# Optimization experiments

Measured on AMD Instinct MI355X. Metric: run time of the kernel, lower is better.

The kernel has to match this reference:

```python
import jax, jax.numpy as jnp
import numpy as np

# ---- config (YOLOv4-style, TRAIN_SIZE=608, P2..P5) ----
STRIDES = (4.0, 8.0, 16.0, 32.0)
ANCHORS = np.array([
    [[12, 16], [19, 36], [40, 28], [36, 75]],
    [[36, 75], [76, 55], [72, 146], [142, 110]],
    [[72, 146], [142, 110], [192, 243], [459, 401]],
    [[142, 110], [192, 243], [300, 300], [459, 401]],
], dtype=np.float32)  # [LEVELS, NUM_ANCHORS, 2]
MAX_PROP = 100
SCORE_THRESH = 0.25
IOU_THRESH = 0.5


def decode_prediction(p, anchors, stride):
    # p: [b, A, h, w, 6] -> [b, A*h*w, 5] with xyxy + score
    b, A, h, w, _ = p.shape
    txy, twh, conf, cls = p[..., :2], p[..., 2:4], p[..., 4:5], p[..., 5:6]
    gx, gy = jnp.meshgrid(jnp.arange(w, dtype=p.dtype), jnp.arange(h, dtype=p.dtype))
    grid = jnp.stack([gx, gy], axis=-1)[None, None]  # [1,1,h,w,2]
    xy = (jax.nn.sigmoid(txy) + grid) * stride
    wh = jnp.exp(twh) * anchors[None, :, None, None, :]
    score = jax.nn.sigmoid(conf) * jax.nn.sigmoid(cls)
    x1y1 = xy - 0.5 * wh
    x2y2 = xy + 0.5 * wh
    out = jnp.concatenate([x1y1, x2y2, score], axis=-1)  # [b,A,h,w,5]
    return out.reshape(b, A * h * w, 5)


def _iou_one_vs_all(box, boxes):
    # box: [4], boxes: [N,4] (xyxy)
    lt = jnp.maximum(box[:2], boxes[:, :2])
    rb = jnp.minimum(box[2:], boxes[:, 2:])
    wh = jnp.maximum(rb - lt, 0.0)
    inter = wh[:, 0] * wh[:, 1]
    a1 = jnp.maximum(box[2] - box[0], 0.0) * jnp.maximum(box[3] - box[1], 0.0)
    a2 = jnp.maximum(boxes[:, 2] - boxes[:, 0], 0.0) * jnp.maximum(boxes[:, 3] - boxes[:, 1], 0.0)
    return inter / (a1 + a2 - inter + 1e-9)


def _nms_single(boxes, scores):
    # greedy NMS, padded to MAX_PROP with zero rows
    s0 = jnp.where(scores >= SCORE_THRESH, scores, 0.0)

    def step(s, _):
        i = jnp.argmax(s)
        sc = s[i]
        box = boxes[i]
        keep = sc > 0.0
        row = jnp.where(keep, jnp.concatenate([box, sc[None]]), jnp.zeros(5, boxes.dtype))
        iou = _iou_one_vs_all(box, boxes)
        s = jnp.where((iou > IOU_THRESH) & keep, 0.0, s)
        s = s.at[i].set(0.0)
        return s, row

    _, props = jax.lax.scan(step, s0, None, length=MAX_PROP)
    return props  # [MAX_PROP, 5]


def entry_stop_gradients(t, mask):
    # gradient flows only through entries where mask==1
    return jax.lax.stop_gradient(t) * (1.0 - mask) + t * mask


def _forward(p2, p3, p4, p5):
    anchors = jnp.asarray(ANCHORS)
    d2 = decode_prediction(p2, anchors[0], STRIDES[0])
    d3 = decode_prediction(p3, anchors[1], STRIDES[1])
    d4 = decode_prediction(p4, anchors[2], STRIDES[2])
    d5 = decode_prediction(p5, anchors[3], STRIDES[3])
    proposals = jnp.concatenate([d2, d3, d4, d5], axis=1)  # [b, N, 5]
    proposals = jax.vmap(lambda pr: _nms_single(pr[:, :4], pr[:, 4]))(proposals)  # [b, MAX_PROP, 5]
    mask = (jnp.sum(proposals[..., :4], axis=-1) != 0.0).astype(proposals.dtype)[..., None]
    return entry_stop_gradients(proposals, mask)


def setup_inputs() -> dict:
    key = jax.random.key(0)
    k2, k3, k4, k5 = jax.random.split(key, 4)
    b, A, ch = 32, 4, 6
    return {
        "p2": jax.random.normal(k2, (b, A, 152, 152, ch), dtype=jnp.float32),
        "p3": jax.random.normal(k3, (b, A, 76, 76, ch), dtype=jnp.float32),
        "p4": jax.random.normal(k4, (b, A, 38, 38, ch), dtype=jnp.float32),
        "p5": jax.random.normal(k5, (b, A, 19, 19, ch), dtype=jnp.float32),
    }


def reference(p2, p3, p4, p5):
    return _forward(p2, p3, p4, p5)
```

## Files before the change

### kernel.cpp

```cpp
#include <hip/hip_runtime.h>
#include <cstdint>
#include <cstddef>

typedef unsigned int u32;
typedef unsigned long long u64;

#define NTOT 122740
#define NPAIR 61370
#define KTOP 1024
#define WIN  256
#define NBIN 4096
#define SCORE_T 0.25f
#define TBITS 0x3E800000u
#define HSPLIT_BITS 0x3EFFF000u
#define CSTRIDE 64
#define CAP_H 40960
#define CAP_L 20480

#define F4TOT 184110
#define F4B3 138624
#define F4B4 173280
#define F4B5 181944

#define WS_SORTED 8192
#define WS_CANDH  270336
#define WS_CANDL  10756096

__device__ __forceinline__ float sigm(float x) { return 1.0f / (1.0f + expf(-x)); }

__device__ __forceinline__ int score_bin(u32 bits) {
  return min(4095, 1 + (int)((bits - TBITS) >> 12));
}

__device__ __forceinline__ u64 shfl_u64(u64 x, int src) {
  int lo = __shfl((int)(u32)x, src, 64);
  int hi = __shfl((int)(u32)(x >> 32), src, 64);
  return ((u64)(u32)hi << 32) | (u32)lo;
}

__device__ __forceinline__ void score_pair(int P, int b,
    const float* __restrict__ p2, const float* __restrict__ p3,
    const float* __restrict__ p4, const float* __restrict__ p5,
    u32& b0, u32& b1, u32& gi0, u32& gi1)
{
  int t0 = 2 * P;
  const float* p; int l0, LN;
  if (t0 < 92416)       { p = p2; l0 = t0;          LN = 92416; }
  else if (t0 < 115520) { p = p3; l0 = t0 - 92416;  LN = 23104; }
  else if (t0 < 121296) { p = p4; l0 = t0 - 115520; LN = 5776;  }
  else                  { p = p5; l0 = t0 - 121296; LN = 1444;  }
  const float* q = p + ((size_t)b * LN + (size_t)l0) * 6;
  float4 v1 = *(const float4*)(q + 4);
  float4 v2 = *(const float4*)(q + 8);
  float s0 = sigm(v1.x) * sigm(v1.y);
  float s1 = sigm(v2.z) * sigm(v2.w);
  b0 = (s0 >= SCORE_T) ? __float_as_uint(s0) : 0u;
  b1 = (s1 >= SCORE_T) ? __float_as_uint(s1) : 0u;
  gi0 = (u32)t0; gi1 = (u32)(t0 + 1);
}

__device__ float4 decode_box_from_gidx(u32 gidx, int b,
    const float* __restrict__ p2, const float* __restrict__ p3,
    const float* __restrict__ p4, const float* __restrict__ p5)
{
  const float* p; int t, H, W; float stride;
  float aw0, ah0, aw1, ah1, aw2, ah2, aw3, ah3;
  if (gidx < 92416u) {
    p = p2 + (size_t)b * 92416 * 6; t = (int)gidx; H = 152; W = 152; stride = 4.0f;
    aw0=12.f; ah0=16.f; aw1=19.f; ah1=36.f; aw2=40.f; ah2=28.f; aw3=36.f; ah3=75.f;
  } else if (gidx < 115520u) {
    p = p3 + (size_t)b * 23104 * 6; t = (int)(gidx - 92416u); H = 76; W = 76; stride = 8.0f;
    aw0=36.f; ah0=75.f; aw1=76.f; ah1=55.f; aw2=72.f; ah2=146.f; aw3=142.f; ah3=110.f;
  } else if (gidx < 121296u) {
    p = p4 + (size_t)b * 5776 * 6; t = (int)(gidx - 115520u); H = 38; W = 38; stride = 16.0f;
    aw0=72.f; ah0=146.f; aw1=142.f; ah1=110.f; aw2=192.f; ah2=243.f; aw3=459.f; ah3=401.f;
  } else {
    p = p5 + (size_t)b * 1444 * 6; t = (int)(gidx - 121296u); H = 19; W = 19; stride = 32.0f;
    aw0=142.f; ah0=110.f; aw1=192.f; ah1=243.f; aw2=300.f; ah2=300.f; aw3=459.f; ah3=401.f;
  }
  int HW = H * W;
  int a = t / HW;
  int r = t - a * HW;
  int y = r / W;
  int x = r - y * W;
  const float* q = p + (size_t)t * 6;
  float2 t01 = *(const float2*)(q + 0);
  float2 t23 = *(const float2*)(q + 2);
  float cx = (sigm(t01.x) + (float)x) * stride;
  float cy = (sigm(t01.y) + (float)y) * stride;
  float aw = (a == 0) ? aw0 : (a == 1) ? aw1 : (a == 2) ? aw2 : aw3;
  float ah = (a == 0) ? ah0 : (a == 1) ? ah1 : (a == 2) ? ah2 : ah3;
  float bw = expf(t23.x) * aw;
  float bh = expf(t23.y) * ah;
  return make_float4(cx - 0.5f * bw, cy - 0.5f * bh, cx + 0.5f * bw, cy + 0.5f * bh);
}

__device__ __forceinline__ bool iou_gt(float4 A, float4 B) {
  float ltx = fmaxf(A.x, B.x), lty = fmaxf(A.y, B.y);
  float rbx = fminf(A.z, B.z), rby = fminf(A.w, B.w);
  float w = fmaxf(rbx - ltx, 0.0f), h = fmaxf(rby - lty, 0.0f);
  float inter = w * h;
  float a1 = fmaxf(A.z - A.x, 0.0f) * fmaxf(A.w - A.y, 0.0f);
  float a2 = fmaxf(B.z - B.x, 0.0f) * fmaxf(B.w - B.y, 0.0f);
  float iou = inter / (a1 + a2 - inter + 1e-9f);
  return iou > 0.5f;
}

__global__ __launch_bounds__(256)
void decode_kernel(const float* __restrict__ p2, const float* __restrict__ p3,
                   const float* __restrict__ p4, const float* __restrict__ p5,
                   u32* __restrict__ counters,
                   uint2* __restrict__ candH, uint2* __restrict__ candL)
{
  __shared__ float4 sbuf4[768];
  __shared__ uint2 stH[512];
  __shared__ uint2 stL[512];
  __shared__ u32 s_cH, s_cL, s_bH, s_bL;
  const int tid = threadIdx.x;
  const int b = blockIdx.y;
  if (tid == 0) { s_cH = 0u; s_cL = 0u; }

  const float4* q2 = (const float4*)p2;
  const float4* q3 = (const float4*)p3;
  const float4* q4 = (const float4*)p4;
  const float4* q5 = (const float4*)p5;

  const int f4base = blockIdx.x * 768;
  #pragma unroll
  for (int j = 0; j < 3; ++j) {
    int idx4 = f4base + j * 256 + tid;
    if (idx4 < F4TOT) {
      const float4* src;
      if (idx4 < F4B3)      src = q2 + (size_t)b * 138624 + idx4;
      else if (idx4 < F4B4) src = q3 + (size_t)b * 34656  + (idx4 - F4B3);
      else if (idx4 < F4B5) src = q4 + (size_t)b * 8664   + (idx4 - F4B4);
      else                  src = q5 + (size_t)b * 2166   + (idx4 - F4B5);
      sbuf4[j * 256 + tid] = *src;
    }
  }
  __syncthreads();

  const float* sbuf = (const float*)sbuf4;
  const int rbase = blockIdx.x * 512;
  #pragma unroll
  for (int k = 0; k < 2; ++k) {
    int lr = 2 * tid + k;
    int rg = rbase + lr;
    if (rg < NTOT) {
      float2 cc = *(const float2*)&sbuf[lr * 6 + 4];
      float s = sigm(cc.x) * sigm(cc.y);
      if (s >= SCORE_T) {
        u32 bits = __float_as_uint(s);
        bool H = (bits >= HSPLIT_BITS);
        u32 pos = atomicAdd(H ? &s_cH : &s_cL, 1u);
        if (pos < 512u) (H ? stH : stL)[pos] = make_uint2(bits, (u32)rg);
      }
    }
  }
  __syncthreads();
  if (tid == 0) {
    if (s_cH) s_bH = atomicAdd(&counters[(size_t)b * CSTRIDE],     s_cH);
    if (s_cL) s_bL = atomicAdd(&counters[(size_t)b * CSTRIDE + 1], s_cL);
  }
  __syncthreads();
  uint2* gH = candH + (size_t)b * CAP_H;
  uint2* gL = candL + (size_t)b * CAP_L;
  const u32 mH = min(s_cH, 512u), mL = min(s_cL, 512u);
  for (u32 i = tid; i < mH; i += 256) { u32 d = s_bH + i; if (d < (u32)CAP_H) gH[d] = stH[i]; }
  for (u32 i = tid; i < mL; i += 256) { u32 d = s_bL + i; if (d < (u32)CAP_L) gL[d] = stL[i]; }
}

__global__ __launch_bounds__(1024, 1)
void sort_kernel(const u32* __restrict__ counters_in, u32* __restrict__ counters,
                 const uint2* __restrict__ candH, const uint2* __restrict__ candL,
                 const float* __restrict__ p2, const float* __restrict__ p3,
                 const float* __restrict__ p4, const float* __restrict__ p5,
                 u64* __restrict__ sortedK)
{
  const int b = blockIdx.x;
  const int tid = threadIdx.x;

  __shared__ u32 sstart[NBIN];
  __shared__ u32 scur[NBIN];
  __shared__ u64 skey[KTOP];
  __shared__ int s_B, s_n;

  const u32 nHc = counters_in[(size_t)b * CSTRIDE];
  const u32 nLc = counters_in[(size_t)b * CSTRIDE + 1];
  const bool readL = (nHc < (u32)KTOP);
  const bool fb = (nHc > (u32)CAP_H) || (readL && nLc > (u32)CAP_L);

  for (int i = tid; i < NBIN; i += 1024) scur[i] = 0u;
  __syncthreads();

  if (!fb) {
    const uint2* gH = candH + (size_t)b * CAP_H;
    for (u32 i = tid; i < nHc; i += 1024) atomicAdd(&scur[score_bin(gH[i].x)], 1u);
    if (readL) {
      const uint2* gL = candL + (size_t)b * CAP_L;
      for (u32 i = tid; i < nLc; i += 1024) atomicAdd(&scur[score_bin(gL[i].x)], 1u);
    }
  } else {
    for (int P = tid; P < NPAIR; P += 1024) {
      u32 b0, b1, gi0, gi1;
      score_pair(P, b, p2, p3, p4, p5, b0, b1, gi0, gi1);
      if (b0) atomicAdd(&scur[score_bin(b0)], 1u);
      if (b1) atomicAdd(&scur[score_bin(b1)], 1u);
    }
  }
  __syncthreads();

  if (tid < 64) {
    u32 h[64];
    #pragma unroll
    for (int k = 0; k < 64; ++k) h[k] = scur[tid * 64 + k];
    u32 lsum = 0;
    #pragma unroll
    for (int k = 0; k < 64; ++k) lsum += h[k];
    u32 S = lsum;
    #pragma unroll
    for (int off = 1; off < 64; off <<= 1) {
      u32 v = (u32)__shfl_down((int)S, off, 64);
      if (tid + off < 64) S += v;
    }
    u32 c = S - lsum;
    int Bv = -1; u32 nv = 0;
    for (int k = 63; k >= 0; --k) {
      sstart[tid * 64 + k] = c;
      c += h[k];
      if (c <= (u32)KTOP) { Bv = tid * 64 + k; nv = c; }
    }
    u32 pk = (Bv < 0) ? 0xFFFFFFFFu : (((u32)Bv << 12) | nv);
    #pragma unroll
    for (int off = 32; off >= 1; off >>= 1) {
      u32 o = (u32)__shfl_down((int)pk, off, 64);
      if (tid + off < 64) pk = min(pk, o);
    }
    if (tid == 0) {
      if (pk == 0xFFFFFFFFu) { s_B = 4095; s_n = KTOP; }
      else { s_B = max((int)(pk >> 12), 1); s_n = (int)(pk & 0xFFFu); }
    }
  }
  __syncthreads();
  const int B = s_B;
  const int n = min(s_n, KTOP);

  for (int i = tid; i < NBIN; i += 1024) scur[i] = sstart[i];
  __syncthreads();

  if (!fb) {
    const uint2* gH = candH + (size_t)b * CAP_H;
    for (u32 i = tid; i < nHc; i += 1024) {
      uint2 e = gH[i];
      int bin = score_bin(e.x);
      if (bin >= B) {
        u32 slot = atomicAdd(&scur[bin], 1u);
        if (slot < (u32)KTOP) skey[slot] = ((u64)e.x << 32) | (u32)(~e.y);
      }
    }
    if (readL) {
      const uint2* gL = candL + (size_t)b * CAP_L;
      for (u32 i = tid; i < nLc; i += 1024) {
        uint2 e = gL[i];
        int bin = score_bin(e.x);
        if (bin >= B) {
          u32 slot = atomicAdd(&scur[bin], 1u);
          if (slot < (u32)KTOP) skey[slot] = ((u64)e.x << 32) | (u32)(~e.y);
        }
      }
    }
  } else {
    for (int P = tid; P < NPAIR; P += 1024) {
      u32 b0, b1, gi0, gi1;
      score_pair(P, b, p2, p3, p4, p5, b0, b1, gi0, gi1);
      if (b0) { int bin = score_bin(b0);
        if (bin >= B) { u32 slot = atomicAdd(&scur[bin], 1u);
          if (slot < (u32)KTOP) skey[slot] = ((u64)b0 << 32) | (u32)(~gi0); } }
      if (b1) { int bin = score_bin(b1);
        if (bin >= B) { u32 slot = atomicAdd(&scur[bin], 1u);
          if (slot < (u32)KTOP) skey[slot] = ((u64)b1 << 32) | (u32)(~gi1); } }
    }
  }
  __syncthreads();

  u64* dst = sortedK + (size_t)b * KTOP;
  for (int s = tid; s < n; s += 1024) {
    u64 k = skey[s];
    int bin = score_bin((u32)(k >> 32));
    int st = (int)sstart[bin];
    int en = (int)scur[bin];
    u32 r = 0;
    for (int j = st; j < en; ++j) r += (skey[j] > k) ? 1u : 0u;
    dst[st + r] = k;
  }
  if (tid == 0) counters[(size_t)b * CSTRIDE + 8] = (u32)n;
}

__global__ __launch_bounds__(1024, 1)
void nms_kernel(const u32* __restrict__ counters, const u64* __restrict__ sortedK,
                const float* __restrict__ p2, const float* __restrict__ p3,
                const float* __restrict__ p4, const float* __restrict__ p5,
                float* __restrict__ out)
{
  const int b = blockIdx.x;
  const int tid = threadIdx.x;

  __shared__ u64 skeyw[WIN];
  __shared__ float4 sbox[WIN];
  __shared__ u64 smat[WIN * 4];
  __shared__ float4 selbox[100];
  __shared__ int s_misc[4];

  const int n = min((int)counters[(size_t)b * CSTRIDE + 8], KTOP);
  const u64* src = sortedK + (size_t)b * KTOP;
  const int Wn = min(n, WIN);

  if (tid < WIN) {
    u64 k = (tid < Wn) ? src[tid] : 0ull;
    skeyw[tid] = k;
    sbox[tid] = (tid < Wn) ? decode_box_from_gidx(~(u32)k, b, p2, p3, p4, p5)
                           : make_float4(0.f, 0.f, 0.f, 0.f);
  }
  __syncthreads();

  {
    int row = tid & 255, word = tid >> 8;
    u64 bits = 0;
    if (row < Wn) {
      float4 A = sbox[row];
      int j0 = word * 64;
      int je = min(64, Wn - j0);
      for (int j = 0; j < je; ++j)
        if (iou_gt(A, sbox[j0 + j])) bits |= (1ull << j);
    }
    smat[word * 256 + row] = bits;
  }
  __syncthreads();

  if (tid < 64) {
    const int lane = tid;
    u64 m0[4], m1[4], m2[4], m3[4];
    #pragma unroll
    for (int w = 0; w < 4; ++w) {
      m0[w] = smat[w * 256 +   0 + lane];
      m1[w] = smat[w * 256 +  64 + lane];
      m2[w] = smat[w * 256 + 128 + lane];
      m3[w] = smat[w * 256 + 192 + lane];
    }
    u64 live[4];
    #pragma unroll
    for (int g2 = 0; g2 < 4; ++g2) {
      int lo = g2 * 64;
      live[g2] = (Wn >= lo + 64) ? ~0ull : (Wn > lo ? ((1ull << (Wn - lo)) - 1ull) : 0ull);
    }
    int sel = 0;
    #pragma unroll 1
    for (int w2 = 0; w2 < 4; ++w2) {
      while (live[w2] && sel < 100) {
        int j = (int)__ffsll(live[w2]) - 1;
        int p = (w2 << 6) + j;
        u64 r0, r1, r2, r3;
        if (w2 == 0)      { r0 = shfl_u64(m0[0], j); r1 = shfl_u64(m0[1], j); r2 = shfl_u64(m0[2], j); r3 = shfl_u64(m0[3], j); }
        else if (w2 == 1) { r0 = shfl_u64(m1[0], j); r1 = shfl_u64(m1[1], j); r2 = shfl_u64(m1[2], j); r3 = shfl_u64(m1[3], j); }
        else if (w2 == 2) { r0 = shfl_u64(m2[0], j); r1 = shfl_u64(m2[1], j); r2 = shfl_u64(m2[2], j); r3 = shfl_u64(m2[3], j); }
        else              { r0 = shfl_u64(m3[0], j); r1 = shfl_u64(m3[1], j); r2 = shfl_u64(m3[2], j); r3 = shfl_u64(m3[3], j); }
        live[0] &= ~r0; live[1] &= ~r1; live[2] &= ~r2; live[3] &= ~r3;
        live[w2] &= ~(1ull << j);
        if (lane == 0) {
          float4 box = sbox[p];
          u64 k = skeyw[p];
          float sc = __uint_as_float((u32)(k >> 32));
          selbox[sel] = box;
          float* orow = out + (size_t)b * 500 + (size_t)sel * 5;
          orow[0] = box.x; orow[1] = box.y; orow[2] = box.z; orow[3] = box.w; orow[4] = sc;
        }
        sel++;
      }
    }
    if (lane == 0) {
      s_misc[2] = sel;
      s_misc[3] = (sel < 100 && n > WIN) ? 1 : 0;
    }
  }
  __syncthreads();

  if (s_misc[3]) {
    if (tid < 64) {
      const int lane = tid;
      int sel = s_misc[2];
      for (int p = WIN; p < n && sel < 100; ++p) {
        u64 k = src[p];
        float4 box = decode_box_from_gidx(~(u32)k, b, p2, p3, p4, p5);
        bool hit = false;
        if (lane < sel) hit = iou_gt(selbox[lane], box);
        if (lane + 64 < sel) hit = hit || iou_gt(selbox[lane + 64], box);
        u64 anyhit = __ballot(hit);
        if (anyhit == 0ull) {
          if (lane == 0) {
            selbox[sel] = box;
            float sc = __uint_as_float((u32)(k >> 32));
            float* orow = out + (size_t)b * 500 + (size_t)sel * 5;
            orow[0] = box.x; orow[1] = box.y; orow[2] = box.z; orow[3] = box.w; orow[4] = sc;
          }
          sel++;
        }
      }
      if (lane == 0) s_misc[2] = sel;
    }
  }
  __syncthreads();

  const int nsel = s_misc[2];
  for (int i = tid; i < (100 - nsel) * 5; i += 1024)
    out[(size_t)b * 500 + (size_t)nsel * 5 + i] = 0.0f;
}

extern "C" void kernel_launch(void* const* d_in, const int* in_sizes, int n_in,
                              void* d_out, int out_size, void* d_ws, size_t ws_size,
                              hipStream_t stream) {
  const float* p2 = (const float*)d_in[0];
  const float* p3 = (const float*)d_in[1];
  const float* p4 = (const float*)d_in[2];
  const float* p5 = (const float*)d_in[3];
  float* out = (float*)d_out;

  unsigned char* w = (unsigned char*)d_ws;
  u32*   counters = (u32*)w;
  u64*   sortedK  = (u64*)(w + WS_SORTED);
  uint2* candH    = (uint2*)(w + WS_CANDH);
  uint2* candL    = (uint2*)(w + WS_CANDL);

  hipMemsetAsync(counters, 0, 32 * CSTRIDE * sizeof(u32), stream);
  decode_kernel<<<dim3(240, 32), 256, 0, stream>>>(p2, p3, p4, p5,
                                                   counters, candH, candL);
  sort_kernel<<<32, 1024, 0, stream>>>(counters, counters, candH, candL,
                                       p2, p3, p4, p5, sortedK);
  nms_kernel<<<32, 1024, 0, stream>>>(counters, sortedK, p2, p3, p4, p5, out);
}
```

Baseline: 188.3 us.

## Fuse sort and NMS kernels, bucket candidates into five score ranges

Merges the sort and NMS kernels into one per-batch kernel that keeps the sorted top-K keys in shared memory, which removes a launch and the global round trip for the sorted keys. The decode kernel now buckets passing candidates into five score ranges with separate counters and capacities, so the sort stage reads only as many ranges as it needs to reach the top-K. Decode blocks grow to 512 threads and stage candidates grouped by range. The costs are more shared memory in the fused kernel and possibly more frequent fallback to full recompute if a range overflows its smaller cap.

```diff
diff --git a/kernel.cpp b/kernel.cpp
--- a/kernel.cpp
+++ b/kernel.cpp
@@ -12,19 +12,31 @@
 #define NBIN 4096
 #define SCORE_T 0.25f
 #define TBITS 0x3E800000u
-#define HSPLIT_BITS 0x3EFFF000u
-#define CSTRIDE 64
-#define CAP_H 40960
-#define CAP_L 20480
+
+#define RT0 0x3F5DF000u
+#define RT1 0x3F3FF000u
+#define RT2 0x3F1FF000u
+#define RT3 0x3EFFF000u
+
+#define CSTRIDE 128
+#define CAP0 4096
+#define CAP1 8192
+#define CAP2 12288
+#define CAP3 16384
+#define CAP4 16384
+#define OFF0 0
+#define OFF1 4096
+#define OFF2 12288
+#define OFF3 24576
+#define OFF4 40960
+#define BATCH_ENT 57344
 
 #define F4TOT 184110
 #define F4B3 138624
 #define F4B4 173280
 #define F4B5 181944
 
-#define WS_SORTED 8192
-#define WS_CANDH  270336
-#define WS_CANDL  10756096
+#define WS_CAND 16384
 
 __device__ __forceinline__ float sigm(float x) { return 1.0f / (1.0f + expf(-x)); }
 
@@ -106,76 +118,97 @@
   return iou > 0.5f;
 }
 
-__global__ __launch_bounds__(256)
+__global__ __launch_bounds__(512)
 void decode_kernel(const float* __restrict__ p2, const float* __restrict__ p3,
                    const float* __restrict__ p4, const float* __restrict__ p5,
-                   u32* __restrict__ counters,
-                   uint2* __restrict__ candH, uint2* __restrict__ candL)
+                   u32* __restrict__ counters, uint2* __restrict__ cand)
 {
-  __shared__ float4 sbuf4[768];
-  __shared__ uint2 stH[512];
-  __shared__ uint2 stL[512];
-  __shared__ u32 s_cH, s_cL, s_bH, s_bL;
+  __shared__ float4 sbuf4[1536];
+  __shared__ uint2 stg[1024];
+  __shared__ u32 lcnt[8], lseg[8], lrank[8], gbase[8];
   const int tid = threadIdx.x;
   const int b = blockIdx.y;
-  if (tid == 0) { s_cH = 0u; s_cL = 0u; }
-
+  if (tid < 8) { lcnt[tid] = 0u; lrank[tid] = 0u; gbase[tid] = 0u; }
+
+  const int rbase = blockIdx.x * 1024;
+  const int FS = blockIdx.x * 1536;
   const float4* q2 = (const float4*)p2;
   const float4* q3 = (const float4*)p3;
   const float4* q4 = (const float4*)p4;
   const float4* q5 = (const float4*)p5;
-
-  const int f4base = blockIdx.x * 768;
   #pragma unroll
   for (int j = 0; j < 3; ++j) {
-    int idx4 = f4base + j * 256 + tid;
+    int idx4 = FS + j * 512 + tid;
     if (idx4 < F4TOT) {
       const float4* src;
       if (idx4 < F4B3)      src = q2 + (size_t)b * 138624 + idx4;
       else if (idx4 < F4B4) src = q3 + (size_t)b * 34656  + (idx4 - F4B3);
       else if (idx4 < F4B5) src = q4 + (size_t)b * 8664   + (idx4 - F4B4);
       else                  src = q5 + (size_t)b * 2166   + (idx4 - F4B5);
-      sbuf4[j * 256 + tid] = *src;
+      sbuf4[j * 512 + tid] = *src;
     }
   }
   __syncthreads();
 
   const float* sbuf = (const float*)sbuf4;
-  const int rbase = blockIdx.x * 512;
+  u32 kb[2]; u32 kg[2]; int kr[2];
   #pragma unroll
   for (int k = 0; k < 2; ++k) {
-    int lr = 2 * tid + k;
+    kb[k] = 0u; kr[k] = -1;
+    int lr = tid + k * 512;
     int rg = rbase + lr;
+    kg[k] = (u32)rg;
     if (rg < NTOT) {
       float2 cc = *(const float2*)&sbuf[lr * 6 + 4];
       float s = sigm(cc.x) * sigm(cc.y);
       if (s >= SCORE_T) {
-        u32 bits = __float_as_uint(s);
-        bool H = (bits >= HSPLIT_BITS);
-        u32 pos = atomicAdd(H ? &s_cH : &s_cL, 1u);
-        if (pos < 512u) (H ? stH : stL)[pos] = make_uint2(bits, (u32)rg);
+        u32 bb = __float_as_uint(s);
+        kb[k] = bb;
+        int r;
+        if      (bb >= RT0) r = 0;
+        else if (bb >= RT1) r = 1;
+        else if (bb >= RT2) r = 2;
+        else if (bb >= RT3) r = 3;
+        else                r = 4;
+        kr[k] = r;
+        atomicAdd(&lcnt[r], 1u);
       }
     }
   }
   __syncthreads();
   if (tid == 0) {
-    if (s_cH) s_bH = atomicAdd(&counters[(size_t)b * CSTRIDE],     s_cH);
-    if (s_cL) s_bL = atomicAdd(&counters[(size_t)b * CSTRIDE + 1], s_cL);
-  }
-  __syncthreads();
-  uint2* gH = candH + (size_t)b * CAP_H;
-  uint2* gL = candL + (size_t)b * CAP_L;
-  const u32 mH = min(s_cH, 512u), mL = min(s_cL, 512u);
-  for (u32 i = tid; i < mH; i += 256) { u32 d = s_bH + i; if (d < (u32)CAP_H) gH[d] = stH[i]; }
-  for (u32 i = tid; i < mL; i += 256) { u32 d = s_bL + i; if (d < (u32)CAP_L) gL[d] = stL[i]; }
+    u32 s = 0;
+    #pragma unroll
+    for (int r = 0; r < 5; ++r) { lseg[r] = s; s += lcnt[r]; }
+  }
+  if (tid < 5 && lcnt[tid]) gbase[tid] = atomicAdd(&counters[(size_t)b * CSTRIDE + tid * 16], lcnt[tid]);
+  __syncthreads();
+  #pragma unroll
+  for (int k = 0; k < 2; ++k) {
+    if (kr[k] >= 0) {
+      u32 rk = atomicAdd(&lrank[kr[k]], 1u);
+      stg[lseg[kr[k]] + rk] = make_uint2(kb[k], kg[k]);
+    }
+  }
+  __syncthreads();
+  uint2* cb = cand + (size_t)b * BATCH_ENT;
+  const u32 roff[5] = { OFF0, OFF1, OFF2, OFF3, OFF4 };
+  const u32 rcap[5] = { CAP0, CAP1, CAP2, CAP3, CAP4 };
+  #pragma unroll
+  for (int r = 0; r < 5; ++r) {
+    const u32 cnt = lcnt[r], sg = lseg[r], gb = gbase[r];
+    for (u32 i = tid; i < cnt; i += 512) {
+      u32 d = gb + i;
+      if (d < rcap[r]) cb[roff[r] + d] = stg[sg + i];
+    }
+  }
 }
 
 __global__ __launch_bounds__(1024, 1)
-void sort_kernel(const u32* __restrict__ counters_in, u32* __restrict__ counters,
-                 const uint2* __restrict__ candH, const uint2* __restrict__ candL,
+void mega_kernel(const u32* __restrict__ counters, const uint2* __restrict__ cand,
                  const float* __restrict__ p2, const float* __restrict__ p3,
                  const float* __restrict__ p4, const float* __restrict__ p5,
-                 u64* __restrict__ sortedK)
+                 float* __restrict__ out)
 {
   const int b = blockIdx.x;
   const int tid = threadIdx.x;
@@ -183,23 +216,44 @@
   __shared__ u32 sstart[NBIN];
   __shared__ u32 scur[NBIN];
   __shared__ u64 skey[KTOP];
+  __shared__ u64 skey2[KTOP];
+  __shared__ float4 sbox[WIN];
+  __shared__ u64 smat[WIN * 4];
+  __shared__ float4 selbox[100];
+  __shared__ int s_misc[4];
   __shared__ int s_B, s_n;
 
-  const u32 nHc = counters_in[(size_t)b * CSTRIDE];
-  const u32 nLc = counters_in[(size_t)b * CSTRIDE + 1];
-  const bool readL = (nHc < (u32)KTOP);
-  const bool fb = (nHc > (u32)CAP_H) || (readL && nLc > (u32)CAP_L);
+  const u32 c0 = counters[(size_t)b * CSTRIDE +  0];
+  const u32 c1 = counters[(size_t)b * CSTRIDE + 16];
+  const u32 c2 = counters[(size_t)b * CSTRIDE + 32];
+  const u32 c3 = counters[(size_t)b * CSTRIDE + 48];
+  const u32 c4 = counters[(size_t)b * CSTRIDE + 64];
+  const u32 total = c0 + c1 + c2 + c3 + c4;
+  const u32 need = min((u32)KTOP, total);
+  int RL = 0;
+  { u32 cum = c0;
+    if (cum < need) { RL = 1; cum += c1; }
+    if (cum < need) { RL = 2; cum += c2; }
+    if (cum < need) { RL = 3; cum += c3; }
+    if (cum < need) { RL = 4; cum += c4; }
+  }
+  const bool fb = (c0 > (u32)CAP0)
+               || (RL >= 1 && c1 > (u32)CAP1)
+               || (RL >= 2 && c2 > (u32)CAP2)
+               || (RL >= 3 && c3 > (u32)CAP3)
+               || (RL >= 4 && c4 > (u32)CAP4);
 
   for (int i = tid; i < NBIN; i += 1024) scur[i] = 0u;
   __syncthreads();
 
+  const uint2* cb = cand + (size_t)b * BATCH_ENT;
+
   if (!fb) {
-    const uint2* gH = candH + (size_t)b * CAP_H;
-    for (u32 i = tid; i < nHc; i += 1024) atomicAdd(&scur[score_bin(gH[i].x)], 1u);
-    if (readL) {
-      const uint2* gL = candL + (size_t)b * CAP_L;
-      for (u32 i = tid; i < nLc; i += 1024) atomicAdd(&scur[score_bin(gL[i].x)], 1u);
-    }
+    for (u32 i = tid; i < c0; i += 1024) atomicAdd(&scur[score_bin(cb[OFF0 + i].x)], 1u);
+    if (RL >= 1) for (u32 i = tid; i < c1; i += 1024) atomicAdd(&scur[score_bin(cb[OFF1 + i].x)], 1u);
+    if (RL >= 2) for (u32 i = tid; i < c2; i += 1024) atomicAdd(&scur[score_bin(cb[OFF2 + i].x)], 1u);
+    if (RL >= 3) for (u32 i = tid; i < c3; i += 1024) atomicAdd(&scur[score_bin(cb[OFF3 + i].x)], 1u);
+    if (RL >= 4) for (u32 i = tid; i < c4; i += 1024) atomicAdd(&scur[score_bin(cb[OFF4 + i].x)], 1u);
   } else {
     for (int P = tid; P < NPAIR; P += 1024) {
       u32 b0, b1, gi0, gi1;
@@ -249,41 +303,45 @@
   __syncthreads();
 
   if (!fb) {
-    const uint2* gH = candH + (size_t)b * CAP_H;
-    for (u32 i = tid; i < nHc; i += 1024) {
-      uint2 e = gH[i];
-      int bin = score_bin(e.x);
-      if (bin >= B) {
-        u32 slot = atomicAdd(&scur[bin], 1u);
-        if (slot < (u32)KTOP) skey[slot] = ((u64)e.x << 32) | (u32)(~e.y);
-      }
-    }
-    if (readL) {
-      const uint2* gL = candL + (size_t)b * CAP_L;
-      for (u32 i = tid; i < nLc; i += 1024) {
-        uint2 e = gL[i];
-        int bin = score_bin(e.x);
-        if (bin >= B) {
-          u32 slot = atomicAdd(&scur[bin], 1u);
-          if (slot < (u32)KTOP) skey[slot] = ((u64)e.x << 32) | (u32)(~e.y);
-        }
-      }
+    for (u32 i = tid; i < c0; i += 1024) {
+      uint2 e = cb[OFF0 + i]; int bin = score_bin(e.x);
+      if (bin >= B) { u32 sl = atomicAdd(&scur[bin], 1u);
+        if (sl < (u32)KTOP) skey[sl] = ((u64)e.x << 32) | (u32)(~e.y); }
+    }
+    if (RL >= 1) for (u32 i = tid; i < c1; i += 1024) {
+      uint2 e = cb[OFF1 + i]; int bin = score_bin(e.x);
+      if (bin >= B) { u32 sl = atomicAdd(&scur[bin], 1u);
+        if (sl < (u32)KTOP) skey[sl] = ((u64)e.x << 32) | (u32)(~e.y); }
+    }
+    if (RL >= 2) for (u32 i = tid; i < c2; i += 1024) {
+      uint2 e = cb[OFF2 + i]; int bin = score_bin(e.x);
+      if (bin >= B) { u32 sl = atomicAdd(&scur[bin], 1u);
+        if (sl < (u32)KTOP) skey[sl] = ((u64)e.x << 32) | (u32)(~e.y); }
+    }
+    if (RL >= 3) for (u32 i = tid; i < c3; i += 1024) {
+      uint2 e = cb[OFF3 + i]; int bin = score_bin(e.x);
+      if (bin >= B) { u32 sl = atomicAdd(&scur[bin], 1u);
+        if (sl < (u32)KTOP) skey[sl] = ((u64)e.x << 32) | (u32)(~e.y); }
+    }
+    if (RL >= 4) for (u32 i = tid; i < c4; i += 1024) {
+      uint2 e = cb[OFF4 + i]; int bin = score_bin(e.x);
+      if (bin >= B) { u32 sl = atomicAdd(&scur[bin], 1u);
+        if (sl < (u32)KTOP) skey[sl] = ((u64)e.x << 32) | (u32)(~e.y); }
     }
   } else {
     for (int P = tid; P < NPAIR; P += 1024) {
       u32 b0, b1, gi0, gi1;
       score_pair(P, b, p2, p3, p4, p5, b0, b1, gi0, gi1);
       if (b0) { int bin = score_bin(b0);
-        if (bin >= B) { u32 slot = atomicAdd(&scur[bin], 1u);
-          if (slot < (u32)KTOP) skey[slot] = ((u64)b0 << 32) | (u32)(~gi0); } }
+        if (bin >= B) { u32 sl = atomicAdd(&scur[bin], 1u);
+          if (sl < (u32)KTOP) skey[sl] = ((u64)b0 << 32) | (u32)(~gi0); } }
       if (b1) { int bin = score_bin(b1);
-        if (bin >= B) { u32 slot = atomicAdd(&scur[bin], 1u);
-          if (slot < (u32)KTOP) skey[slot] = ((u64)b1 << 32) | (u32)(~gi1); } }
-    }
-  }
-  __syncthreads();
-
-  u64* dst = sortedK + (size_t)b * KTOP;
+        if (bin >= B) { u32 sl = atomicAdd(&scur[bin], 1u);
+          if (sl < (u32)KTOP) skey[sl] = ((u64)b1 << 32) | (u32)(~gi1); } }
+    }
+  }
+  __syncthreads();
+
   for (int s = tid; s < n; s += 1024) {
     u64 k = skey[s];
     int bin = score_bin((u32)(k >> 32));
@@ -291,34 +349,14 @@
     int en = (int)scur[bin];
     u32 r = 0;
     for (int j = st; j < en; ++j) r += (skey[j] > k) ? 1u : 0u;
-    dst[st + r] = k;
-  }
-  if (tid == 0) counters[(size_t)b * CSTRIDE + 8] = (u32)n;
-}
-
-__global__ __launch_bounds__(1024, 1)
-void nms_kernel(const u32* __restrict__ counters, const u64* __restrict__ sortedK,
-                const float* __restrict__ p2, const float* __restrict__ p3,
-                const float* __restrict__ p4, const float* __restrict__ p5,
-                float* __restrict__ out)
-{
-  const int b = blockIdx.x;
-  const int tid = threadIdx.x;
-
-  __shared__ u64 skeyw[WIN];
-  __shared__ float4 sbox[WIN];
-  __shared__ u64 smat[WIN * 4];
-  __shared__ float4 selbox[100];
-  __shared__ int s_misc[4];
-
-  const int n = min((int)counters[(size_t)b * CSTRIDE + 8], KTOP);
-  const u64* src = sortedK + (size_t)b * KTOP;
+    skey2[st + r] = k;
+  }
+  __syncthreads();
+
   const int Wn = min(n, WIN);
 
   if (tid < WIN) {
-    u64 k = (tid < Wn) ? src[tid] : 0ull;
-    skeyw[tid] = k;
-    sbox[tid] = (tid < Wn) ? decode_box_from_gidx(~(u32)k, b, p2, p3, p4, p5)
+    sbox[tid] = (tid < Wn) ? decode_box_from_gidx(~(u32)skey2[tid], b, p2, p3, p4, p5)
                            : make_float4(0.f, 0.f, 0.f, 0.f);
   }
   __syncthreads();
@@ -368,7 +406,7 @@
         live[w2] &= ~(1ull << j);
         if (lane == 0) {
           float4 box = sbox[p];
-          u64 k = skeyw[p];
+          u64 k = skey2[p];
           float sc = __uint_as_float((u32)(k >> 32));
           selbox[sel] = box;
           float* orow = out + (size_t)b * 500 + (size_t)sel * 5;
@@ -389,7 +427,7 @@
       const int lane = tid;
       int sel = s_misc[2];
       for (int p = WIN; p < n && sel < 100; ++p) {
-        u64 k = src[p];
+        u64 k = skey2[p];
         float4 box = decode_box_from_gidx(~(u32)k, b, p2, p3, p4, p5);
         bool hit = false;
         if (lane < sel) hit = iou_gt(selbox[lane], box);
@@ -426,14 +464,9 @@
 
   unsigned char* w = (unsigned char*)d_ws;
   u32*   counters = (u32*)w;
-  u64*   sortedK  = (u64*)(w + WS_SORTED);
-  uint2* candH    = (uint2*)(w + WS_CANDH);
-  uint2* candL    = (uint2*)(w + WS_CANDL);
+  uint2* cand     = (uint2*)(w + WS_CAND);
 
   hipMemsetAsync(counters, 0, 32 * CSTRIDE * sizeof(u32), stream);
-  decode_kernel<<<dim3(240, 32), 256, 0, stream>>>(p2, p3, p4, p5,
-                                                   counters, candH, candL);
-  sort_kernel<<<32, 1024, 0, stream>>>(counters, counters, candH, candL,
-                                       p2, p3, p4, p5, sortedK);
-  nms_kernel<<<32, 1024, 0, stream>>>(counters, sortedK, p2, p3, p4, p5, out);
-}
+  decode_kernel<<<dim3(120, 32), 512, 0, stream>>>(p2, p3, p4, p5, counters, cand);
+  mega_kernel<<<32, 1024, 0, stream>>>(counters, cand, p2, p3, p4, p5, out);
+}
```

Measured after the change: 176.2 us. -6.4%, faster.
